# Kernel optimization log

Measured on AMD Instinct MI355X. Metric: run time of the kernel, lower is better.

The kernel has to match this reference:

```python
import jax, jax.numpy as jnp
import numpy as np

B, S, D, H, DH = 4, 2048, 1024, 16, 64

def setup_inputs() -> dict:
    key = jax.random.key(0)
    k1, k2, k3, k4, k5 = jax.random.split(key, 5)
    scale = 1.0 / np.sqrt(D)
    return {
        "x": jax.random.normal(k1, (B, S, D), dtype=jnp.float32),
        "w_qkv": jax.random.normal(k2, (D, 3, H, DH), dtype=jnp.float32) * scale,
        "b_qkv": jax.random.normal(k3, (3, H, DH), dtype=jnp.float32) * 0.02,
        "w_out": jax.random.normal(k4, (H, DH, D), dtype=jnp.float32) * (1.0 / np.sqrt(H * DH)),
        "b_out": jax.random.normal(k5, (D,), dtype=jnp.float32) * 0.02,
    }

def reference(x, w_qkv, b_qkv, w_out, b_out):
    # QKV projection: [B,S,D] x [D,3,H,Dh] -> [B,S,3,H,Dh]
    qkv = jnp.einsum('bsd,dthe->bsthe', x, w_qkv) + b_qkv
    q, k, v = qkv[:, :, 0], qkv[:, :, 1], qkv[:, :, 2]  # each [B,S,H,Dh]
    head_dim = q.shape[-1]
    # scores [B,H,Sq,Sk]
    scores = jnp.einsum('bqhe,bkhe->bhqk', q, k) / jnp.sqrt(jnp.float32(head_dim))
    seq = scores.shape[-1]
    causal = (jnp.arange(seq)[:, None] >= jnp.arange(seq)[None, :]).astype(scores.dtype)
    scores = scores - 1e9 * (1.0 - causal)  # additive mask as in source
    weights = jax.nn.softmax(scores, axis=-1)
    # dropout inactive (inference=True default)
    answers = jnp.einsum('bhqk,bkhe->bqhe', weights, v)  # [B,S,H,Dh]
    out = jnp.einsum('bqhe,hed->bqd', answers, w_out) + b_out
    return out
```

## Files before the change

### kernel.cpp

```cpp
#include <hip/hip_runtime.h>
#include <hip/hip_bf16.h>
#include <stdint.h>

#define B_    4
#define S_    2048
#define D_    1024
#define H_    16
#define DH_   64
#define M_TOT 8192
#define NQKV  3072
#define HDH   1024

typedef __bf16 bf16_t;
typedef bf16_t bf16x8 __attribute__((ext_vector_type(8)));
typedef float  f32x4  __attribute__((ext_vector_type(4)));
typedef float  f32x16 __attribute__((ext_vector_type(16)));

#define QSCALE 0.1803368801111204f

__device__ __forceinline__ short f2bf(float f) {
  union { float f; uint32_t u; } x; x.f = f;
  uint32_t r = (x.u + 0x7fffu + ((x.u >> 16) & 1u)) >> 16;
  return (short)(uint16_t)r;
}

__device__ __forceinline__ uint32_t cvt_pk_bf16(float lo, float hi) {
  uint32_t r;
  asm("v_cvt_pk_bf16_f32 %0, %1, %2" : "=v"(r) : "v"(lo), "v"(hi));
  return r;
}

__device__ __forceinline__ void permlane32_swap(uint32_t& d, uint32_t& s) {
  asm("v_permlane32_swap_b32 %0, %1" : "+v"(d), "+v"(s));
}

#define ASYNC_COPY16(g, l) \
  __builtin_amdgcn_global_load_lds((const __attribute__((address_space(1))) void*)(g), \
                                   (__attribute__((address_space(3))) void*)(l), 16, 0, 0)


__global__ __launch_bounds__(256) void k_cvt(const float* __restrict__ in, short* __restrict__ out, int n4) {
  int i = blockIdx.x * 256 + threadIdx.x;
  if (i < n4) {
    float4 v = ((const float4*)in)[i];
    short4 o;
    o.x = f2bf(v.x); o.y = f2bf(v.y); o.z = f2bf(v.z); o.w = f2bf(v.w);
    ((short4*)out)[i] = o;
  }
}

__global__ __launch_bounds__(256) void k_transpose_t(const float* __restrict__ in, short* __restrict__ out,
                                                     int R, int C) {
  __shared__ short t[32][33];
  const int bx = blockIdx.x * 32;
  const int by = blockIdx.y * 32;
  const int tid = threadIdx.x;
  const int row = tid >> 3, c4 = (tid & 7) * 4;
  const float4 v = *(const float4*)&in[(size_t)(by + row) * C + bx + c4];
  t[row][c4 + 0] = f2bf(v.x); t[row][c4 + 1] = f2bf(v.y);
  t[row][c4 + 2] = f2bf(v.z); t[row][c4 + 3] = f2bf(v.w);
  __syncthreads();
  short4 o;
  o.x = t[c4 + 0][row]; o.y = t[c4 + 1][row];
  o.z = t[c4 + 2][row]; o.w = t[c4 + 3][row];
  *(short4*)&out[(size_t)(bx + row) * R + by + c4] = o;
}


__device__ __forceinline__ void gemm_core(const short* __restrict__ A,
                                          const short* __restrict__ Bt,
                                          int row0, int col0, int K,
                                          short* lA, short* lB,
                                          f32x4 acc[4][4]) {
  const int tid  = threadIdx.x;
  const int wave = tid >> 6, lane = tid & 63;
  const int wr = wave >> 1, wc = wave & 1;
  const int stg_r = lane >> 2;
  const int stg_k = (lane & 3) * 8;
  const int fr = lane & 15;
  const int fk = (lane >> 4) * 8;

  for (int k0 = 0; k0 < K; k0 += 32) {
    __syncthreads();
#pragma unroll
    for (int c = 0; c < 2; ++c) {
      const int seg = wave * 2 + c;
      const short* ga = A  + (size_t)(row0 + seg * 16 + stg_r) * K + (k0 + stg_k);
      const short* gb = Bt + (size_t)(col0 + seg * 16 + stg_r) * K + (k0 + stg_k);
      ASYNC_COPY16(ga, lA + seg * 512);
      ASYNC_COPY16(gb, lB + seg * 512);
    }
    __syncthreads();
    bf16x8 af[4], bfr[4];
#pragma unroll
    for (int m = 0; m < 4; ++m)
      af[m] = *(const bf16x8*)(lA + (wr * 64 + m * 16 + fr) * 32 + fk);
#pragma unroll
    for (int n = 0; n < 4; ++n)
      bfr[n] = *(const bf16x8*)(lB + (wc * 64 + n * 16 + fr) * 32 + fk);
#pragma unroll
    for (int m = 0; m < 4; ++m)
#pragma unroll
      for (int n = 0; n < 4; ++n)
        acc[m][n] = __builtin_amdgcn_mfma_f32_16x16x32_bf16(af[m], bfr[n], acc[m][n], 0, 0, 0);
  }
}

__global__ __launch_bounds__(256) void k_gemm_qkv(const short* __restrict__ A, const short* __restrict__ Bt,
                                                  const float* __restrict__ bias,
                                                  short* __restrict__ Qb, short* __restrict__ Kb,
                                                  short* __restrict__ Vt) {
  __shared__ short lA[128 * 32];
  __shared__ short lB[128 * 32];
  f32x4 acc[4][4];
#pragma unroll
  for (int m = 0; m < 4; ++m)
#pragma unroll
    for (int n = 0; n < 4; ++n)
      acc[m][n] = (f32x4){0.f, 0.f, 0.f, 0.f};
  const int row0 = blockIdx.x * 128, col0 = blockIdx.y * 128;
  gemm_core(A, Bt, row0, col0, D_, lA, lB, acc);
  const int lane = threadIdx.x & 63, wave = threadIdx.x >> 6;
  const int wr = wave >> 1, wc = wave & 1;
#pragma unroll
  for (int m = 0; m < 4; ++m) {
    const int rbase = row0 + wr * 64 + m * 16 + (lane >> 4) * 4;
#pragma unroll
    for (int n = 0; n < 4; ++n) {
      const int col = col0 + wc * 64 + n * 16 + (lane & 15);
      const float bv = bias[col];
      const int t = col >> 10, rem = col & 1023, hh = rem >> 6, e = rem & 63;
#pragma unroll
      for (int r = 0; r < 4; ++r) {
        const int rw = rbase + r;
        const int bb = rw >> 11, s = rw & 2047;
        float v = acc[m][n][r] + bv;
        if (t == 0) {
          Qb[((size_t)(bb * H_ + hh) * S_ + s) * DH_ + e] = f2bf(v * QSCALE);
        } else if (t == 1) {
          Kb[((size_t)(bb * H_ + hh) * S_ + s) * DH_ + e] = f2bf(v);
        } else {
          Vt[((size_t)(bb * H_ + hh) * DH_ + e) * S_ + s] = f2bf(v);
        }
      }
    }
  }
}

__global__ __launch_bounds__(256) void k_gemm_out(const short* __restrict__ A, const short* __restrict__ Bt,
                                                  const float* __restrict__ bias, float* __restrict__ C) {
  __shared__ short lA[128 * 32];
  __shared__ short lB[128 * 32];
  f32x4 acc[4][4];
#pragma unroll
  for (int m = 0; m < 4; ++m)
#pragma unroll
    for (int n = 0; n < 4; ++n)
      acc[m][n] = (f32x4){0.f, 0.f, 0.f, 0.f};
  const int row0 = blockIdx.x * 128, col0 = blockIdx.y * 128;
  gemm_core(A, Bt, row0, col0, HDH, lA, lB, acc);
  const int lane = threadIdx.x & 63, wave = threadIdx.x >> 6;
  const int wr = wave >> 1, wc = wave & 1;
#pragma unroll
  for (int m = 0; m < 4; ++m) {
    const int rbase = row0 + wr * 64 + m * 16 + (lane >> 4) * 4;
#pragma unroll
    for (int n = 0; n < 4; ++n) {
      const int col = col0 + wc * 64 + n * 16 + (lane & 15);
      const float bv = bias[col];
#pragma unroll
      for (int r = 0; r < 4; ++r)
        C[(size_t)(rbase + r) * D_ + col] = acc[m][n][r] + bv;
    }
  }
}


template <bool MASKED>
__device__ __forceinline__ void softmax_pack(const f32x16& sacc, int ql, int hi,
                                             f32x16& o0, f32x16& o1,
                                             float& m, float& lsum,
                                             bf16x8& pb0v, bf16x8& pb1v) {
  float p[16];
#pragma unroll
  for (int r = 0; r < 16; ++r) {
    float s = sacc[r];
    if (MASKED) {
      const int kl = (r & 3) + 8 * (r >> 2) + 4 * hi;
      s = (kl <= ql) ? s : -1.0e30f;
    }
    p[r] = s;
  }
  float t0 = fmaxf(fmaxf(p[0], p[1]), p[2]);
  float t1 = fmaxf(fmaxf(p[3], p[4]), p[5]);
  float t2 = fmaxf(fmaxf(p[6], p[7]), p[8]);
  float t3 = fmaxf(fmaxf(p[9], p[10]), p[11]);
  float t4 = fmaxf(fmaxf(p[12], p[13]), p[14]);
  float pmax = fmaxf(fmaxf(fmaxf(t0, t1), t2), fmaxf(fmaxf(t3, t4), p[15]));
  if (__any(pmax - m > 8.0f)) {
    const float pmr = fmaxf(pmax, __shfl_xor(pmax, 32));
    const float mn = fmaxf(m, pmr);
    const float al = __builtin_amdgcn_exp2f(m - mn);
    lsum *= al;
#pragma unroll
    for (int r = 0; r < 16; ++r) { o0[r] *= al; o1[r] *= al; }
    m = mn;
  }
#pragma unroll
  for (int r = 0; r < 16; ++r) p[r] = __builtin_amdgcn_exp2f(p[r] - m);
  {
    float s0 = (p[0] + p[1]) + (p[2] + p[3]);
    float s1 = (p[4] + p[5]) + (p[6] + p[7]);
    float s2 = (p[8] + p[9]) + (p[10] + p[11]);
    float s3 = (p[12] + p[13]) + (p[14] + p[15]);
    lsum += (s0 + s1) + (s2 + s3);
  }
  uint32_t A0 = cvt_pk_bf16(p[0],  p[1]);
  uint32_t A1 = cvt_pk_bf16(p[2],  p[3]);
  uint32_t B0 = cvt_pk_bf16(p[4],  p[5]);
  uint32_t B1 = cvt_pk_bf16(p[6],  p[7]);
  uint32_t A2 = cvt_pk_bf16(p[8],  p[9]);
  uint32_t A3 = cvt_pk_bf16(p[10], p[11]);
  uint32_t B2 = cvt_pk_bf16(p[12], p[13]);
  uint32_t B3 = cvt_pk_bf16(p[14], p[15]);
  permlane32_swap(A0, B0);
  permlane32_swap(A1, B1);
  permlane32_swap(A2, B2);
  permlane32_swap(A3, B3);
  union { uint32_t u[4]; bf16x8 v; } pb0, pb1;
  pb0.u[0] = A0; pb0.u[1] = A1; pb0.u[2] = B0; pb0.u[3] = B1;
  pb1.u[0] = A2; pb1.u[1] = A3; pb1.u[2] = B2; pb1.u[3] = B3;
  pb0v = pb0.v; pb1v = pb1.v;
}

template <bool MASKED>
__device__ __forceinline__ void attn_tile(int kt, int ql, int hi,
                                          const short* __restrict__ Kp,
                                          const short* __restrict__ Vp,
                                          const bf16x8 qf[4],
                                          f32x16& oacc0, f32x16& oacc1,
                                          float& m, float& lsum) {
  const short* kb = Kp + (size_t)(kt + ql) * DH_ + hi * 8;
  bf16x8 kf0 = *(const bf16x8*)(kb);
  bf16x8 kf1 = *(const bf16x8*)(kb + 16);
  bf16x8 kf2 = *(const bf16x8*)(kb + 32);
  bf16x8 kf3 = *(const bf16x8*)(kb + 48);
  const short* vb0 = Vp + (size_t)(ql) * S_ + kt + hi * 8;
  const short* vb1 = Vp + (size_t)(32 + ql) * S_ + kt + hi * 8;
  bf16x8 vf00 = *(const bf16x8*)(vb0);
  bf16x8 vf01 = *(const bf16x8*)(vb0 + 16);
  bf16x8 vf10 = *(const bf16x8*)(vb1);
  bf16x8 vf11 = *(const bf16x8*)(vb1 + 16);

  f32x16 sacc;
#pragma unroll
  for (int r = 0; r < 16; ++r) sacc[r] = 0.f;
  sacc = __builtin_amdgcn_mfma_f32_32x32x16_bf16(kf0, qf[0], sacc, 0, 0, 0);
  sacc = __builtin_amdgcn_mfma_f32_32x32x16_bf16(kf1, qf[1], sacc, 0, 0, 0);
  sacc = __builtin_amdgcn_mfma_f32_32x32x16_bf16(kf2, qf[2], sacc, 0, 0, 0);
  sacc = __builtin_amdgcn_mfma_f32_32x32x16_bf16(kf3, qf[3], sacc, 0, 0, 0);

  bf16x8 pb0, pb1;
  softmax_pack<MASKED>(sacc, ql, hi, oacc0, oacc1, m, lsum, pb0, pb1);

  oacc0 = __builtin_amdgcn_mfma_f32_32x32x16_bf16(vf00, pb0, oacc0, 0, 0, 0);
  oacc0 = __builtin_amdgcn_mfma_f32_32x32x16_bf16(vf01, pb1, oacc0, 0, 0, 0);
  oacc1 = __builtin_amdgcn_mfma_f32_32x32x16_bf16(vf10, pb0, oacc1, 0, 0, 0);
  oacc1 = __builtin_amdgcn_mfma_f32_32x32x16_bf16(vf11, pb1, oacc1, 0, 0, 0);
}

template <bool MASKA>
__device__ __forceinline__ void attn_tile2(int kt, int ql, int hi,
                                           const short* __restrict__ Kp,
                                           const short* __restrict__ Vp,
                                           const bf16x8 qfA[4], const bf16x8 qfB[4],
                                           f32x16& oA0, f32x16& oA1, float& mA, float& lA,
                                           f32x16& oB0, f32x16& oB1, float& mB, float& lB) {
  const short* kb = Kp + (size_t)(kt + ql) * DH_ + hi * 8;
  bf16x8 kf0 = *(const bf16x8*)(kb);
  bf16x8 kf1 = *(const bf16x8*)(kb + 16);
  bf16x8 kf2 = *(const bf16x8*)(kb + 32);
  bf16x8 kf3 = *(const bf16x8*)(kb + 48);
  const short* vb0 = Vp + (size_t)(ql) * S_ + kt + hi * 8;
  const short* vb1 = Vp + (size_t)(32 + ql) * S_ + kt + hi * 8;
  bf16x8 vf00 = *(const bf16x8*)(vb0);
  bf16x8 vf01 = *(const bf16x8*)(vb0 + 16);
  bf16x8 vf10 = *(const bf16x8*)(vb1);
  bf16x8 vf11 = *(const bf16x8*)(vb1 + 16);

  f32x16 sA, sB;
#pragma unroll
  for (int r = 0; r < 16; ++r) { sA[r] = 0.f; sB[r] = 0.f; }
  sA = __builtin_amdgcn_mfma_f32_32x32x16_bf16(kf0, qfA[0], sA, 0, 0, 0);
  sB = __builtin_amdgcn_mfma_f32_32x32x16_bf16(kf0, qfB[0], sB, 0, 0, 0);
  sA = __builtin_amdgcn_mfma_f32_32x32x16_bf16(kf1, qfA[1], sA, 0, 0, 0);
  sB = __builtin_amdgcn_mfma_f32_32x32x16_bf16(kf1, qfB[1], sB, 0, 0, 0);
  sA = __builtin_amdgcn_mfma_f32_32x32x16_bf16(kf2, qfA[2], sA, 0, 0, 0);
  sB = __builtin_amdgcn_mfma_f32_32x32x16_bf16(kf2, qfB[2], sB, 0, 0, 0);
  sA = __builtin_amdgcn_mfma_f32_32x32x16_bf16(kf3, qfA[3], sA, 0, 0, 0);
  sB = __builtin_amdgcn_mfma_f32_32x32x16_bf16(kf3, qfB[3], sB, 0, 0, 0);

  bf16x8 pA0, pA1, pB0, pB1;
  softmax_pack<MASKA>(sA, ql, hi, oA0, oA1, mA, lA, pA0, pA1);
  softmax_pack<false>(sB, ql, hi, oB0, oB1, mB, lB, pB0, pB1);

  oA0 = __builtin_amdgcn_mfma_f32_32x32x16_bf16(vf00, pA0, oA0, 0, 0, 0);
  oB0 = __builtin_amdgcn_mfma_f32_32x32x16_bf16(vf00, pB0, oB0, 0, 0, 0);
  oA0 = __builtin_amdgcn_mfma_f32_32x32x16_bf16(vf01, pA1, oA0, 0, 0, 0);
  oB0 = __builtin_amdgcn_mfma_f32_32x32x16_bf16(vf01, pB1, oB0, 0, 0, 0);
  oA1 = __builtin_amdgcn_mfma_f32_32x32x16_bf16(vf10, pA0, oA1, 0, 0, 0);
  oB1 = __builtin_amdgcn_mfma_f32_32x32x16_bf16(vf10, pB0, oB1, 0, 0, 0);
  oA1 = __builtin_amdgcn_mfma_f32_32x32x16_bf16(vf11, pA1, oA1, 0, 0, 0);
  oB1 = __builtin_amdgcn_mfma_f32_32x32x16_bf16(vf11, pB1, oB1, 0, 0, 0);
}

__device__ __forceinline__ void write_out(short* __restrict__ att, int b, int h,
                                          int q0, int ql, int hi,
                                          const f32x16& o0, const f32x16& o1, float lsum) {
  lsum += __shfl_xor(lsum, 32);
  const float rl = __builtin_amdgcn_rcpf(lsum);
  short* ob = att + (size_t)((size_t)b * S_ + q0 + ql) * HDH + h * DH_ + 4 * hi;
#pragma unroll
  for (int dt = 0; dt < 2; ++dt) {
#pragma unroll
    for (int a = 0; a < 4; ++a) {
      const int rb = 4 * a;
      float v0 = (dt ? o1[rb + 0] : o0[rb + 0]) * rl;
      float v1 = (dt ? o1[rb + 1] : o0[rb + 1]) * rl;
      float v2 = (dt ? o1[rb + 2] : o0[rb + 2]) * rl;
      float v3 = (dt ? o1[rb + 3] : o0[rb + 3]) * rl;
      short4 o;
      o.x = f2bf(v0); o.y = f2bf(v1); o.z = f2bf(v2); o.w = f2bf(v3);
      *(short4*)(ob + dt * 32 + 8 * a) = o;
    }
  }
}

__global__ __launch_bounds__(64, 3) void k_attn(const short* __restrict__ Qb, const short* __restrict__ Kb,
                                                const short* __restrict__ Vt, short* __restrict__ att) {
  const int lane = threadIdx.x & 63;
  const int j = blockIdx.x;
  const int xcd = j & 7, c = j >> 3;
  const int bhLo = c & 7;
  const int s = 31 - (c >> 3);
  const int gg = xcd + 8 * bhLo;
  const int b = gg >> 4, h = gg & 15;
  const int pA = 2 * s, pB = 2 * s + 1;
  const int qA = pA * 32, qB = pB * 32;
  const size_t bh = (size_t)(b * H_ + h);
  const short* Qp = Qb + bh * (S_ * DH_);
  const short* Kp = Kb + bh * (S_ * DH_);
  const short* Vp = Vt + bh * (DH_ * S_);
  const int ql = lane & 31, hi = lane >> 5;

  bf16x8 qfA[4], qfB[4];
#pragma unroll
  for (int ss = 0; ss < 4; ++ss) {
    qfA[ss] = *(const bf16x8*)(Qp + (size_t)(qA + ql) * DH_ + ss * 16 + hi * 8);
    qfB[ss] = *(const bf16x8*)(Qp + (size_t)(qB + ql) * DH_ + ss * 16 + hi * 8);
  }

  f32x16 oA0, oA1, oB0, oB1;
#pragma unroll
  for (int r = 0; r < 16; ++r) { oA0[r] = 0.f; oA1[r] = 0.f; oB0[r] = 0.f; oB1[r] = 0.f; }
  float mA = -3.0e38f, lA = 0.f, mB = -3.0e38f, lB = 0.f;

#pragma unroll 1
  for (int t = 0; t < pA; ++t)
    attn_tile2<false>(t * 32, ql, hi, Kp, Vp, qfA, qfB, oA0, oA1, mA, lA, oB0, oB1, mB, lB);
  attn_tile2<true>(qA, ql, hi, Kp, Vp, qfA, qfB, oA0, oA1, mA, lA, oB0, oB1, mB, lB);
  attn_tile<true>(qB, ql, hi, Kp, Vp, qfB, oB0, oB1, mB, lB);

  write_out(att, b, h, qA, ql, hi, oA0, oA1, lA);
  write_out(att, b, h, qB, ql, hi, oB0, oB1, lB);
}


extern "C" void kernel_launch(void* const* d_in, const int* in_sizes, int n_in,
                              void* d_out, int out_size, void* d_ws, size_t ws_size,
                              hipStream_t stream) {
  const float* x     = (const float*)d_in[0];
  const float* w_qkv = (const float*)d_in[1];
  const float* b_qkv = (const float*)d_in[2];
  const float* w_out = (const float*)d_in[3];
  const float* b_out = (const float*)d_in[4];
  float* out = (float*)d_out;

  char* p = (char*)d_ws;
  short* xb    = (short*)p; p += (size_t)M_TOT * D_ * 2;
  short* wqkvT = (short*)p; p += (size_t)NQKV * D_ * 2;
  short* woutT = (short*)p; p += (size_t)D_ * HDH * 2;
  short* Qb    = (short*)p; p += (size_t)B_ * H_ * S_ * DH_ * 2;
  short* Kb    = (short*)p; p += (size_t)B_ * H_ * S_ * DH_ * 2;
  short* Vt    = (short*)p; p += (size_t)B_ * H_ * S_ * DH_ * 2;
  short* att   = (short*)p; p += (size_t)M_TOT * HDH * 2;

  k_cvt<<<M_TOT * D_ / 4 / 256, 256, 0, stream>>>(x, xb, M_TOT * D_ / 4);
  k_transpose_t<<<dim3(NQKV / 32, D_ / 32), 256, 0, stream>>>(w_qkv, wqkvT, D_, NQKV);
  k_transpose_t<<<dim3(D_ / 32, HDH / 32), 256, 0, stream>>>(w_out, woutT, HDH, D_);
  k_gemm_qkv<<<dim3(M_TOT / 128, NQKV / 128), 256, 0, stream>>>(xb, wqkvT, b_qkv, Qb, Kb, Vt);
  k_attn<<<2048, 64, 0, stream>>>(Qb, Kb, Vt, att);
  k_gemm_out<<<dim3(M_TOT / 128, D_ / 128), 256, 0, stream>>>(att, woutT, b_out, out);
}
```

Before: 207.8 us.

## Split long causal query tiles into KV chunks with a separate merge kernel

The attention kernel changes from one wave per pair of query tiles to one wave per single query tile. Tiles in the back half of the sequence are split into two KV chunks whose partial outputs, maxima and sums are written to a workspace, and a new merge kernel combines them with log-sum-exp rescaling. The goal is better load balance and more parallelism: the grid grows from 2048 to 6144 waves and occupancy is raised to 6 waves per SIMD. The cost is an extra kernel launch, extra global traffic for the partials, loss of K/V register reuse across two query tiles, and bf16 rounding of the unnormalized partial outputs.

```diff
diff --git a/kernel.cpp b/kernel.cpp
--- a/kernel.cpp
+++ b/kernel.cpp
@@ -22,6 +22,10 @@
   union { float f; uint32_t u; } x; x.f = f;
   uint32_t r = (x.u + 0x7fffu + ((x.u >> 16) & 1u)) >> 16;
   return (short)(uint16_t)r;
+}
+
+__device__ __forceinline__ float bf2f(uint16_t u) {
+  union { uint32_t u; float f; } x; x.u = (uint32_t)u << 16; return x.f;
 }
 
 __device__ __forceinline__ uint32_t cvt_pk_bf16(float lo, float hi) {
@@ -269,110 +273,129 @@
   oacc1 = __builtin_amdgcn_mfma_f32_32x32x16_bf16(vf11, pb1, oacc1, 0, 0, 0);
 }
 
-template <bool MASKA>
-__device__ __forceinline__ void attn_tile2(int kt, int ql, int hi,
-                                           const short* __restrict__ Kp,
-                                           const short* __restrict__ Vp,
-                                           const bf16x8 qfA[4], const bf16x8 qfB[4],
-                                           f32x16& oA0, f32x16& oA1, float& mA, float& lA,
-                                           f32x16& oB0, f32x16& oB1, float& mB, float& lB) {
-  const short* kb = Kp + (size_t)(kt + ql) * DH_ + hi * 8;
-  bf16x8 kf0 = *(const bf16x8*)(kb);
-  bf16x8 kf1 = *(const bf16x8*)(kb + 16);
-  bf16x8 kf2 = *(const bf16x8*)(kb + 32);
-  bf16x8 kf3 = *(const bf16x8*)(kb + 48);
-  const short* vb0 = Vp + (size_t)(ql) * S_ + kt + hi * 8;
-  const short* vb1 = Vp + (size_t)(32 + ql) * S_ + kt + hi * 8;
-  bf16x8 vf00 = *(const bf16x8*)(vb0);
-  bf16x8 vf01 = *(const bf16x8*)(vb0 + 16);
-  bf16x8 vf10 = *(const bf16x8*)(vb1);
-  bf16x8 vf11 = *(const bf16x8*)(vb1 + 16);
-
-  f32x16 sA, sB;
-#pragma unroll
-  for (int r = 0; r < 16; ++r) { sA[r] = 0.f; sB[r] = 0.f; }
-  sA = __builtin_amdgcn_mfma_f32_32x32x16_bf16(kf0, qfA[0], sA, 0, 0, 0);
-  sB = __builtin_amdgcn_mfma_f32_32x32x16_bf16(kf0, qfB[0], sB, 0, 0, 0);
-  sA = __builtin_amdgcn_mfma_f32_32x32x16_bf16(kf1, qfA[1], sA, 0, 0, 0);
-  sB = __builtin_amdgcn_mfma_f32_32x32x16_bf16(kf1, qfB[1], sB, 0, 0, 0);
-  sA = __builtin_amdgcn_mfma_f32_32x32x16_bf16(kf2, qfA[2], sA, 0, 0, 0);
-  sB = __builtin_amdgcn_mfma_f32_32x32x16_bf16(kf2, qfB[2], sB, 0, 0, 0);
-  sA = __builtin_amdgcn_mfma_f32_32x32x16_bf16(kf3, qfA[3], sA, 0, 0, 0);
-  sB = __builtin_amdgcn_mfma_f32_32x32x16_bf16(kf3, qfB[3], sB, 0, 0, 0);
-
-  bf16x8 pA0, pA1, pB0, pB1;
-  softmax_pack<MASKA>(sA, ql, hi, oA0, oA1, mA, lA, pA0, pA1);
-  softmax_pack<false>(sB, ql, hi, oB0, oB1, mB, lB, pB0, pB1);
-
-  oA0 = __builtin_amdgcn_mfma_f32_32x32x16_bf16(vf00, pA0, oA0, 0, 0, 0);
-  oB0 = __builtin_amdgcn_mfma_f32_32x32x16_bf16(vf00, pB0, oB0, 0, 0, 0);
-  oA0 = __builtin_amdgcn_mfma_f32_32x32x16_bf16(vf01, pA1, oA0, 0, 0, 0);
-  oB0 = __builtin_amdgcn_mfma_f32_32x32x16_bf16(vf01, pB1, oB0, 0, 0, 0);
-  oA1 = __builtin_amdgcn_mfma_f32_32x32x16_bf16(vf10, pA0, oA1, 0, 0, 0);
-  oB1 = __builtin_amdgcn_mfma_f32_32x32x16_bf16(vf10, pB0, oB1, 0, 0, 0);
-  oA1 = __builtin_amdgcn_mfma_f32_32x32x16_bf16(vf11, pA1, oA1, 0, 0, 0);
-  oB1 = __builtin_amdgcn_mfma_f32_32x32x16_bf16(vf11, pB1, oB1, 0, 0, 0);
-}
-
-__device__ __forceinline__ void write_out(short* __restrict__ att, int b, int h,
-                                          int q0, int ql, int hi,
-                                          const f32x16& o0, const f32x16& o1, float lsum) {
-  lsum += __shfl_xor(lsum, 32);
-  const float rl = __builtin_amdgcn_rcpf(lsum);
-  short* ob = att + (size_t)((size_t)b * S_ + q0 + ql) * HDH + h * DH_ + 4 * hi;
-#pragma unroll
-  for (int dt = 0; dt < 2; ++dt) {
-#pragma unroll
-    for (int a = 0; a < 4; ++a) {
-      const int rb = 4 * a;
-      float v0 = (dt ? o1[rb + 0] : o0[rb + 0]) * rl;
-      float v1 = (dt ? o1[rb + 1] : o0[rb + 1]) * rl;
-      float v2 = (dt ? o1[rb + 2] : o0[rb + 2]) * rl;
-      float v3 = (dt ? o1[rb + 3] : o0[rb + 3]) * rl;
-      short4 o;
-      o.x = f2bf(v0); o.y = f2bf(v1); o.z = f2bf(v2); o.w = f2bf(v3);
-      *(short4*)(ob + dt * 32 + 8 * a) = o;
-    }
-  }
-}
-
-__global__ __launch_bounds__(64, 3) void k_attn(const short* __restrict__ Qb, const short* __restrict__ Kb,
-                                                const short* __restrict__ Vt, short* __restrict__ att) {
+__global__ __launch_bounds__(64, 6) void k_attn(const short* __restrict__ Qb, const short* __restrict__ Kb,
+                                                const short* __restrict__ Vt, short* __restrict__ att,
+                                                short* __restrict__ Opart, float* __restrict__ Mpart,
+                                                float* __restrict__ Lpart) {
   const int lane = threadIdx.x & 63;
   const int j = blockIdx.x;
   const int xcd = j & 7, c = j >> 3;
-  const int bhLo = c & 7;
-  const int s = 31 - (c >> 3);
+  const int bhLo = c & 7, u = c >> 3;
   const int gg = xcd + 8 * bhLo;
   const int b = gg >> 4, h = gg & 15;
-  const int pA = 2 * s, pB = 2 * s + 1;
-  const int qA = pA * 32, qB = pB * 32;
+
+  int p, t0, chunk;
+  bool has_diag, direct;
+  if (u < 32) {
+    p = 32 + u; t0 = 0; chunk = 0; has_diag = false; direct = false;
+  } else {
+    const int v = u - 32, k = v >> 1;
+    if ((v & 1) == 0) { p = 31 - k; t0 = 0; chunk = 0; has_diag = true; direct = true; }
+    else             { p = 63 - k; t0 = 32; chunk = 1; has_diag = true; direct = false; }
+  }
+  const int cap = has_diag ? p : 32;
+  const int q0 = p * 32;
+
   const size_t bh = (size_t)(b * H_ + h);
   const short* Qp = Qb + bh * (S_ * DH_);
   const short* Kp = Kb + bh * (S_ * DH_);
   const short* Vp = Vt + bh * (DH_ * S_);
   const int ql = lane & 31, hi = lane >> 5;
 
-  bf16x8 qfA[4], qfB[4];
-#pragma unroll
-  for (int ss = 0; ss < 4; ++ss) {
-    qfA[ss] = *(const bf16x8*)(Qp + (size_t)(qA + ql) * DH_ + ss * 16 + hi * 8);
-    qfB[ss] = *(const bf16x8*)(Qp + (size_t)(qB + ql) * DH_ + ss * 16 + hi * 8);
-  }
-
-  f32x16 oA0, oA1, oB0, oB1;
-#pragma unroll
-  for (int r = 0; r < 16; ++r) { oA0[r] = 0.f; oA1[r] = 0.f; oB0[r] = 0.f; oB1[r] = 0.f; }
-  float mA = -3.0e38f, lA = 0.f, mB = -3.0e38f, lB = 0.f;
+  bf16x8 qf[4];
+#pragma unroll
+  for (int ss = 0; ss < 4; ++ss)
+    qf[ss] = *(const bf16x8*)(Qp + (size_t)(q0 + ql) * DH_ + ss * 16 + hi * 8);
+
+  f32x16 o0, o1;
+#pragma unroll
+  for (int r = 0; r < 16; ++r) { o0[r] = 0.f; o1[r] = 0.f; }
+  float m = -3.0e38f, lsum = 0.f;
 
 #pragma unroll 1
-  for (int t = 0; t < pA; ++t)
-    attn_tile2<false>(t * 32, ql, hi, Kp, Vp, qfA, qfB, oA0, oA1, mA, lA, oB0, oB1, mB, lB);
-  attn_tile2<true>(qA, ql, hi, Kp, Vp, qfA, qfB, oA0, oA1, mA, lA, oB0, oB1, mB, lB);
-  attn_tile<true>(qB, ql, hi, Kp, Vp, qfB, oB0, oB1, mB, lB);
-
-  write_out(att, b, h, qA, ql, hi, oA0, oA1, lA);
-  write_out(att, b, h, qB, ql, hi, oB0, oB1, lB);
+  for (int t = t0; t < cap; ++t)
+    attn_tile<false>(t * 32, ql, hi, Kp, Vp, qf, o0, o1, m, lsum);
+  if (has_diag)
+    attn_tile<true>(q0, ql, hi, Kp, Vp, qf, o0, o1, m, lsum);
+
+  lsum += __shfl_xor(lsum, 32);
+
+  if (direct) {
+    const float rl = __builtin_amdgcn_rcpf(lsum);
+    short* ob = att + (size_t)((size_t)b * S_ + q0 + ql) * HDH + h * DH_ + 4 * hi;
+#pragma unroll
+    for (int dt = 0; dt < 2; ++dt) {
+#pragma unroll
+      for (int a = 0; a < 4; ++a) {
+        const int rb = 4 * a;
+        short4 o;
+        o.x = f2bf((dt ? o1[rb + 0] : o0[rb + 0]) * rl);
+        o.y = f2bf((dt ? o1[rb + 1] : o0[rb + 1]) * rl);
+        o.z = f2bf((dt ? o1[rb + 2] : o0[rb + 2]) * rl);
+        o.w = f2bf((dt ? o1[rb + 3] : o0[rb + 3]) * rl);
+        *(short4*)(ob + dt * 32 + 8 * a) = o;
+      }
+    }
+  } else {
+    const int idx = (gg * 32 + (p - 32)) * 2 + chunk;
+    short* opb = Opart + (size_t)idx * 2048 + ql * 64 + 4 * hi;
+#pragma unroll
+    for (int dt = 0; dt < 2; ++dt) {
+#pragma unroll
+      for (int a = 0; a < 4; ++a) {
+        const int rb = 4 * a;
+        short4 o;
+        o.x = f2bf(dt ? o1[rb + 0] : o0[rb + 0]);
+        o.y = f2bf(dt ? o1[rb + 1] : o0[rb + 1]);
+        o.z = f2bf(dt ? o1[rb + 2] : o0[rb + 2]);
+        o.w = f2bf(dt ? o1[rb + 3] : o0[rb + 3]);
+        *(short4*)(opb + dt * 32 + 8 * a) = o;
+      }
+    }
+    if (hi == 0) {
+      Mpart[idx * 32 + ql] = m;
+      Lpart[idx * 32 + ql] = lsum;
+    }
+  }
+}
+
+__global__ __launch_bounds__(256) void k_merge(const short* __restrict__ Opart,
+                                               const float* __restrict__ Mpart,
+                                               const float* __restrict__ Lpart,
+                                               short* __restrict__ att) {
+  const int blk = blockIdx.x;
+  const int gg = blk >> 5, pp = blk & 31;
+  const int b = gg >> 4, h = gg & 15;
+  const int p = 32 + pp, q0 = p * 32;
+  const int idx0 = (gg * 32 + pp) * 2, idx1 = idx0 + 1;
+  const int row = threadIdx.x >> 3;
+  const int dlo = (threadIdx.x & 7) * 8;
+
+  const float m0 = Mpart[idx0 * 32 + row], m1 = Mpart[idx1 * 32 + row];
+  const float M = fmaxf(m0, m1);
+  const float a0 = __builtin_amdgcn_exp2f(m0 - M);
+  const float a1 = __builtin_amdgcn_exp2f(m1 - M);
+  const float L = Lpart[idx0 * 32 + row] * a0 + Lpart[idx1 * 32 + row] * a1;
+  const float rL = __builtin_amdgcn_rcpf(L);
+  const float f0 = a0 * rL, f1 = a1 * rL;
+
+  const short* p0 = Opart + (size_t)idx0 * 2048 + row * 64 + dlo;
+  const short* p1 = Opart + (size_t)idx1 * 2048 + row * 64 + dlo;
+  short4 x0 = *(const short4*)(p0), y0 = *(const short4*)(p0 + 4);
+  short4 x1 = *(const short4*)(p1), y1 = *(const short4*)(p1 + 4);
+  short4 w0, w1;
+  w0.x = f2bf(bf2f((uint16_t)x0.x) * f0 + bf2f((uint16_t)x1.x) * f1);
+  w0.y = f2bf(bf2f((uint16_t)x0.y) * f0 + bf2f((uint16_t)x1.y) * f1);
+  w0.z = f2bf(bf2f((uint16_t)x0.z) * f0 + bf2f((uint16_t)x1.z) * f1);
+  w0.w = f2bf(bf2f((uint16_t)x0.w) * f0 + bf2f((uint16_t)x1.w) * f1);
+  w1.x = f2bf(bf2f((uint16_t)y0.x) * f0 + bf2f((uint16_t)y1.x) * f1);
+  w1.y = f2bf(bf2f((uint16_t)y0.y) * f0 + bf2f((uint16_t)y1.y) * f1);
+  w1.z = f2bf(bf2f((uint16_t)y0.z) * f0 + bf2f((uint16_t)y1.z) * f1);
+  w1.w = f2bf(bf2f((uint16_t)y0.w) * f0 + bf2f((uint16_t)y1.w) * f1);
+
+  short* ob = att + (size_t)((size_t)b * S_ + q0 + row) * HDH + h * DH_ + dlo;
+  *(short4*)(ob)     = w0;
+  *(short4*)(ob + 4) = w1;
 }
 
 
@@ -394,11 +417,15 @@
   short* Kb    = (short*)p; p += (size_t)B_ * H_ * S_ * DH_ * 2;
   short* Vt    = (short*)p; p += (size_t)B_ * H_ * S_ * DH_ * 2;
   short* att   = (short*)p; p += (size_t)M_TOT * HDH * 2;
+  short* Opart = (short*)p; p += (size_t)4096 * 2048 * 2;
+  float* Mpart = (float*)p; p += (size_t)4096 * 32 * 4;
+  float* Lpart = (float*)p; p += (size_t)4096 * 32 * 4;
 
   k_cvt<<<M_TOT * D_ / 4 / 256, 256, 0, stream>>>(x, xb, M_TOT * D_ / 4);
   k_transpose_t<<<dim3(NQKV / 32, D_ / 32), 256, 0, stream>>>(w_qkv, wqkvT, D_, NQKV);
   k_transpose_t<<<dim3(D_ / 32, HDH / 32), 256, 0, stream>>>(w_out, woutT, HDH, D_);
   k_gemm_qkv<<<dim3(M_TOT / 128, NQKV / 128), 256, 0, stream>>>(xb, wqkvT, b_qkv, Qb, Kb, Vt);
-  k_attn<<<2048, 64, 0, stream>>>(Qb, Kb, Vt, att);
+  k_attn<<<6144, 64, 0, stream>>>(Qb, Kb, Vt, att, Opart, Mpart, Lpart);
+  k_merge<<<2048, 256, 0, stream>>>(Opart, Mpart, Lpart, att);
   k_gemm_out<<<dim3(M_TOT / 128, D_ / 128), 256, 0, stream>>>(att, woutT, b_out, out);
 }
```

Result: slower. 325.5 us (+56.6%).
